# Optimization experiments

Hardware: AMD Instinct MI355X
Metric: run time of the kernel (lower is better)

## Reference

```python
import jax, jax.numpy as jnp
import numpy as np

# dims: batch, time grid, encoder length, state(y) ch, control ch (incl. time), hidden, mlp width, out ch
B, T, L_IN, S, XC, H, W, O = 64, 200, 100, 8, 16, 256, 128, 8
N_SUB = 2  # fixed Dopri5 substeps per save interval (replaces diffrax adaptive PID stepping)


def setup_inputs() -> dict:
    key = jax.random.key(0)
    ks = jax.random.split(key, 16)
    rn = lambda k, shp, sc: jax.random.normal(k, shp, dtype=jnp.float32) * sc
    return {
        "y_past": rn(ks[0], (B, L_IN, S), 1.0),
        "t": jnp.linspace(0.0, 2.0, T, dtype=jnp.float32),
        "coeffs_x": rn(ks[1], (B, T, XC - 1), 1.0),
        "gru_wih": rn(ks[2], (3 * H, S + XC), (S + XC) ** -0.5),
        "gru_whh": rn(ks[3], (3 * H, H), H ** -0.5),
        "gru_b": rn(ks[4], (3 * H,), 0.01),
        "gru_bn": rn(ks[5], (H,), 0.01),
        "mlp_w0": rn(ks[6], (W, H), H ** -0.5),
        "mlp_b0": rn(ks[7], (W,), 0.01),
        "mlp_w1": rn(ks[8], (W, W), W ** -0.5),
        "mlp_b1": rn(ks[9], (W,), 0.01),
        "mlp_w2": rn(ks[10], (H * XC, W), W ** -0.5),
        "mlp_b2": rn(ks[11], (H * XC,), 0.01),
        "ro_w": rn(ks[12], (O, H), H ** -0.5),
        "ro_b": rn(ks[13], (O,), 0.01),
        "input_length": L_IN,
    }


def _forward(y_past, t, coeffs_x, gru_wih, gru_whh, gru_b, gru_bn,
             mlp_w0, mlp_b0, mlp_w1, mlp_b1, mlp_w2, mlp_b2, ro_w, ro_b, input_length):
    L = input_length  # static python int

    def gru_cell(x, h):  # equinox GRUCell math
        ig = gru_wih @ x + gru_b
        hg = gru_whh @ h
        ir, iz, ia = jnp.split(ig, 3)
        hr, hz, hn = jnp.split(hg, 3)
        r = jax.nn.sigmoid(ir + hr)
        u = jax.nn.sigmoid(iz + hz)
        n = jnp.tanh(ia + r * (hn + gru_bn))
        return n + u * (h - n)

    def vf(z, dxdt):  # CDEFunc mlp(z).reshape(H, XC) @ dX/dt
        a = jax.nn.softplus(mlp_w0 @ z + mlp_b0)
        a = jax.nn.softplus(mlp_w1 @ a + mlp_b1)
        f = jnp.tanh(mlp_w2 @ a + mlp_b2).reshape(H, XC)
        return f @ dxdt

    def dopri5_step(z, h, dxdt):  # standard Dormand-Prince 5(4) tableau
        k1 = vf(z, dxdt)
        k2 = vf(z + h * (0.2 * k1), dxdt)
        k3 = vf(z + h * (3 / 40 * k1 + 9 / 40 * k2), dxdt)
        k4 = vf(z + h * (44 / 45 * k1 - 56 / 15 * k2 + 32 / 9 * k3), dxdt)
        k5 = vf(z + h * (19372 / 6561 * k1 - 25360 / 2187 * k2 + 64448 / 6561 * k3 - 212 / 729 * k4), dxdt)
        k6 = vf(z + h * (9017 / 3168 * k1 - 355 / 33 * k2 + 46732 / 5247 * k3 + 49 / 176 * k4 - 5103 / 18656 * k5), dxdt)
        return z + h * (35 / 384 * k1 + 500 / 1113 * k3 + 125 / 192 * k4 - 2187 / 6784 * k5 + 11 / 84 * k6)

    def single(y_p, cx):
        X = jnp.concatenate([cx, t[:, None]], axis=1)  # (T, XC): control values = linear interp knots
        enc_in = jnp.concatenate([y_p, X[:L]], axis=1)  # (L, S+XC); control.evaluate at knots == knot values
        z0, _ = jax.lax.scan(lambda h_, x: (gru_cell(x, h_), None),
                             jnp.zeros((H,), dtype=y_p.dtype), enc_in)
        t_fut = t[L:]
        X_fut = X[L:]
        dts = t_fut[1:] - t_fut[:-1]                       # (Tf-1,)
        dXdt = (X_fut[1:] - X_fut[:-1]) / dts[:, None]     # piecewise-constant derivative of linear interp

        def interval(z, inp):
            dxdt, dt_tot = inp
            hstep = dt_tot / N_SUB
            z, _ = jax.lax.scan(lambda zz, _: (dopri5_step(zz, hstep, dxdt), None), z, None, length=N_SUB)
            return z, z

        _, zs = jax.lax.scan(interval, z0, (dXdt, dts))     # (Tf-1, H)
        ys = jnp.concatenate([z0[None], zs], axis=0)        # (Tf, H), saved at t_future
        return ys @ ro_w.T + ro_b                           # readout, (Tf, O)

    return jax.vmap(single)(y_past, coeffs_x)


def reference(y_past, t, coeffs_x, gru_wih, gru_whh, gru_b, gru_bn,
              mlp_w0, mlp_b0, mlp_w1, mlp_b1, mlp_w2, mlp_b2, ro_w, ro_b, input_length):
    return _forward(y_past, t, coeffs_x, gru_wih, gru_whh, gru_b, gru_bn,
                    mlp_w0, mlp_b0, mlp_w1, mlp_b1, mlp_w2, mlp_b2, ro_w, ro_b, input_length)
```

## Files before the change

### kernel.cpp

```cpp
#include <hip/hip_runtime.h>
#include <math.h>

constexpr int B_   = 64;
constexpr int T_   = 200;
constexpr int L_IN = 100;
constexpr int S_   = 8;
constexpr int XC_  = 16;
constexpr int H_   = 256;
constexpr int W_   = 128;
constexpr int O_   = 8;
constexpr int GR_  = 3 * H_;
constexpr int HXC  = H_ * XC_;

constexpr int NB   = 4;
constexpr int ZPB  = 64;
constexpr int SLOT = 128;

#define NT 1024

constexpr size_t OFF_WIHT = 0;
constexpr size_t OFF_WHHT = OFF_WIHT + 24ull * GR_;
constexpr size_t OFF_W2T  = OFF_WHHT + (size_t)H_ * GR_;
constexpr size_t OFF_KX   = OFF_W2T + (size_t)W_ * HXC;
constexpr size_t KX_U64   = (size_t)B_ * 2 * NB * SLOT;
constexpr size_t WS_FLOATS = OFF_KX + KX_U64 * 2;

__global__ void transpose_kernel(const float* __restrict__ in, float* __restrict__ out,
                                 int R, int K) {
    int o = blockIdx.x * blockDim.x + threadIdx.x;
    if (o < R * K) {
        int k = o / R;
        int j = o - k * R;
        out[o] = in[j * K + k];
    }
}

__device__ __forceinline__ float softplus_f(float x) {
    return fmaxf(x, 0.f) + log1pf(expf(-fabsf(x)));
}
__device__ __forceinline__ float sigmoid_f(float x) {
    return 1.f / (1.f + expf(-x));
}

__global__ __launch_bounds__(NT, 4) void gru_cde_dist(
    const float* __restrict__ y_past,
    const float* __restrict__ tvals,
    const float* __restrict__ cx,
    const float* __restrict__ wih,
    const float* __restrict__ whh,
    const float* __restrict__ gru_b,
    const float* __restrict__ gru_bn,
    const float* __restrict__ w0,
    const float* __restrict__ b0,
    const float* __restrict__ w1,
    const float* __restrict__ b1,
    const float* __restrict__ w2T,
    const float* __restrict__ b2,
    const float* __restrict__ ro_w,
    const float* __restrict__ ro_b,
    unsigned long long* __restrict__ kx,
    float* __restrict__ out)
{
    const int b   = blockIdx.x & (B_ - 1);
    const int q   = blockIdx.x >> 6;
    const int tid = threadIdx.x;

    __shared__ __align__(16) float z[H_];
    __shared__ __align__(16) float zsq[ZPB];
    __shared__ float kbq[5][ZPB];
    __shared__ __align__(16) float a0s[W_];
    __shared__ __align__(16) float a1s[W_];
    __shared__ float vown[W_];
    __shared__ __align__(16) float4 red4[4][256];
    __shared__ float gsum[192];
    __shared__ float gaux[ZPB];
    __shared__ __align__(16) float xb[S_ + XC_];
    __shared__ float dxs[XC_];
    __shared__ __align__(16) float4 w2lds[4][8][256];

    int  epoch = 0;
    bool dead  = false;
    float hh   = 0.f;

    auto slotbase = [&](int qq) -> size_t {
        return (((size_t)b * 2 + (epoch & 1)) * NB + qq) * SLOT;
    };
    auto publish_u64 = [&](int elem, float v) {
        unsigned long long pk = ((unsigned long long)(unsigned)epoch << 32)
                              | (unsigned long long)__float_as_uint(v);
        __hip_atomic_store(&kx[slotbase(q) + elem], pk,
                           __ATOMIC_RELAXED, __HIP_MEMORY_SCOPE_AGENT);
    };
    auto poll_u64 = [&](int qq, int elem) -> float {
        unsigned long long pk = 0;
        int guard = 0;
        for (;;) {
            pk = __hip_atomic_load(&kx[slotbase(qq) + elem],
                                   __ATOMIC_RELAXED, __HIP_MEMORY_SCOPE_AGENT);
            if ((unsigned)(pk >> 32) >= (unsigned)epoch) break;
            if (++guard > (1 << 20)) { dead = true; break; }
        }
        return __uint_as_float((unsigned)pk);
    };

    const int   seg = tid >> 6;
    const int   l63 = tid & 63;
    const int   grow = seg * H_ + q * ZPB + l63;
    const float gbr = (tid < 192) ? gru_b[grow] : 0.f;
    const float bnr = (tid < ZPB) ? gru_bn[q * ZPB + tid] : 0.f;

    if (tid < H_) z[tid] = 0.f;
    if (tid < S_ + XC_) {
        float v;
        if (tid < S_)                v = y_past[(b * L_IN) * S_ + tid];
        else if (tid < S_ + XC_ - 1) v = cx[(b * T_) * (XC_ - 1) + (tid - S_)];
        else                         v = tvals[0];
        xb[tid] = v;
    }
    __syncthreads();

    for (int step = 0; step < L_IN; ++step) {
        if (tid < 192) {
            const float4* xr = reinterpret_cast<const float4*>(xb);
            const float4* wr = reinterpret_cast<const float4*>(wih + grow * 24);
            float ig = gbr;
            #pragma unroll
            for (int c = 0; c < 6; ++c) {
                float4 wv = wr[c], xv = xr[c];
                ig += wv.x * xv.x + wv.y * xv.y + wv.z * xv.z + wv.w * xv.w;
            }
            const float4* hr = reinterpret_cast<const float4*>(whh + grow * 256);
            const float4* z4 = reinterpret_cast<const float4*>(z);
            float hg = 0.f, hg2 = 0.f;
            #pragma unroll 8
            for (int c = 0; c < 64; c += 2) {
                float4 wa = hr[c],     za = z4[c];
                float4 wb = hr[c + 1], zb = z4[c + 1];
                hg  += wa.x * za.x + wa.y * za.y + wa.z * za.z + wa.w * za.w;
                hg2 += wb.x * zb.x + wb.y * zb.y + wb.z * zb.z + wb.w * zb.w;
            }
            hg += hg2;
            if (seg < 2) gsum[tid] = ig + hg;
            else { gsum[tid] = ig; gaux[l63] = hg; }
        }
        __syncthreads();
        epoch++;
        if (tid < ZPB) {
            float rr = sigmoid_f(gsum[tid]);
            float uu = sigmoid_f(gsum[64 + tid]);
            float nn = tanhf(gsum[128 + tid] + rr * (gaux[tid] + bnr));
            float zo = z[q * ZPB + tid];
            float znew = nn + uu * (zo - nn);
            z[q * ZPB + tid] = znew;
            publish_u64(tid, znew);
        } else if (tid < 256) {
            if (!dead) {
                int pp = tid >> 6;
                int qq = (q + pp) & 3;
                int e  = tid & 63;
                float v = poll_u64(qq, e);
                z[qq * 64 + e] = v;
            }
        } else if (tid < 256 + S_ + XC_ && step + 1 < L_IN) {
            int c = tid - 256;
            float v;
            if (c < S_)                v = y_past[(b * L_IN + step + 1) * S_ + c];
            else if (c < S_ + XC_ - 1) v = cx[(b * T_ + step + 1) * (XC_ - 1) + (c - S_)];
            else                       v = tvals[step + 1];
            xb[c] = v;
        }
        __syncthreads();
    }

    auto readout = [&](int idx) {
        if (q == 0 && tid < 8 * 64) {
            int o  = tid >> 6;
            int kk = tid & 63;
            float4 wv = reinterpret_cast<const float4*>(ro_w)[o * 64 + kk];
            float4 zv = *reinterpret_cast<const float4*>(&z[kk * 4]);
            float p = wv.x * zv.x + wv.y * zv.y + wv.z * zv.z + wv.w * zv.w;
            p += __shfl_xor(p, 1);
            p += __shfl_xor(p, 2);
            p += __shfl_xor(p, 4);
            p += __shfl_xor(p, 8);
            p += __shfl_xor(p, 16);
            p += __shfl_xor(p, 32);
            if (kk == 0) out[(b * L_IN + idx) * O_ + o] = p + ro_b[o];
        }
    };

    readout(0);

    const int wv_ = tid >> 6;
    const int ln  = tid & 63;
    const int vr  = wv_ * 8 + (ln >> 3);
    const int vc  = ln & 7;
    const int g2  = tid >> 8;
    const int u   = tid & 255;

    const float4* __restrict__ w04  = reinterpret_cast<const float4*>(w0);
    const float4* __restrict__ w14  = reinterpret_cast<const float4*>(w1);
    const float4* __restrict__ w2T4 = reinterpret_cast<const float4*>(w2T);

    const float4 w0r0 = w04[vr * 64 + q * 16 + vc * 2];
    const float4 w0r1 = w04[vr * 64 + q * 16 + vc * 2 + 1];
    const float4 w1r0 = w14[vr * 32 + vc * 4 + 0];
    const float4 w1r1 = w14[vr * 32 + vc * 4 + 1];
    const float4 w1r2 = w14[vr * 32 + vc * 4 + 2];
    const float4 w1r3 = w14[vr * 32 + vc * 4 + 3];
    const size_t w2base = (size_t)g2 * 32 * 1024 + (size_t)q * 256 + u;
    const float4 w2c0 = w2T4[w2base + 0 * 1024];
    const float4 w2c1 = w2T4[w2base + 1 * 1024];
    const float4 w2c2 = w2T4[w2base + 2 * 1024];
    const float4 w2c3 = w2T4[w2base + 3 * 1024];
    const float4 w2c4 = w2T4[w2base + 4 * 1024];
    const float4 w2c5 = w2T4[w2base + 5 * 1024];
    const float4 w2c6 = w2T4[w2base + 6 * 1024];
    const float4 w2c7 = w2T4[w2base + 7 * 1024];
    for (int it = 0; it < 8; ++it) {
        int L   = it * 1024 + tid;
        int g2l = L >> 11;
        int jl  = (L >> 8) & 7;
        int ul  = L & 255;
        w2lds[g2l][jl][ul] =
            w2T4[(size_t)(g2l * 32 + 8 + jl) * 1024 + (size_t)q * 256 + ul];
    }

    const float b0r = (tid < W_) ? b0[tid] : 0.f;
    const float b1r = b1[vr];
    float4 b2c = make_float4(0.f, 0.f, 0.f, 0.f);
    if (tid < 256) b2c = reinterpret_cast<const float4*>(b2)[q * 256 + tid];
    float4 dx4 = make_float4(0.f, 0.f, 0.f, 0.f);
    __syncthreads();

    for (int i = 0; i < T_ - L_IN - 1; ++i) {
        float dt = tvals[L_IN + i + 1] - tvals[L_IN + i];
        hh = dt * 0.5f;
        if (tid < XC_) {
            float xa, xbv;
            if (tid < XC_ - 1) {
                xa  = cx[(b * T_ + L_IN + i) * (XC_ - 1) + tid];
                xbv = cx[(b * T_ + L_IN + i + 1) * (XC_ - 1) + tid];
            } else {
                xa  = tvals[L_IN + i];
                xbv = tvals[L_IN + i + 1];
            }
            dxs[tid] = (xbv - xa) / dt;
        }
        __syncthreads();
        if (tid < 256) {
            int c0 = (tid & 3) * 4;
            dx4 = make_float4(dxs[c0], dxs[c0 + 1], dxs[c0 + 2], dxs[c0 + 3]);
        }

        for (int sub = 0; sub < 2; ++sub) {
            if (tid < ZPB) zsq[tid] = z[q * ZPB + tid];
            __syncthreads();

            for (int s = 0; s < 6; ++s) {
                epoch++;
                {
                    const float* zp = &zsq[vc * 8];
                    float pv = w0r0.x * zp[0] + w0r0.y * zp[1]
                             + w0r0.z * zp[2] + w0r0.w * zp[3]
                             + w0r1.x * zp[4] + w0r1.y * zp[5]
                             + w0r1.z * zp[6] + w0r1.w * zp[7];
                    pv += __shfl_xor(pv, 1);
                    pv += __shfl_xor(pv, 2);
                    pv += __shfl_xor(pv, 4);
                    if ((ln & 7) == 0) {
                        vown[vr] = pv;
                        publish_u64(vr, pv);
                    }
                }
                __syncthreads();
                if (tid < W_) {
                    float gv = vown[tid] + b0r;
                    if (!dead) {
                        const size_t s1 = slotbase((q + 1) & 3) + tid;
                        const size_t s2 = slotbase((q + 2) & 3) + tid;
                        const size_t s3 = slotbase((q + 3) & 3) + tid;
                        unsigned long long p1 = 0, p2 = 0, p3 = 0;
                        bool d1 = false, d2 = false, d3 = false;
                        int guard = 0;
                        do {
                            if (!d1) {
                                p1 = __hip_atomic_load(&kx[s1], __ATOMIC_RELAXED,
                                                       __HIP_MEMORY_SCOPE_AGENT);
                                d1 = (unsigned)(p1 >> 32) >= (unsigned)epoch;
                            }
                            if (!d2) {
                                p2 = __hip_atomic_load(&kx[s2], __ATOMIC_RELAXED,
                                                       __HIP_MEMORY_SCOPE_AGENT);
                                d2 = (unsigned)(p2 >> 32) >= (unsigned)epoch;
                            }
                            if (!d3) {
                                p3 = __hip_atomic_load(&kx[s3], __ATOMIC_RELAXED,
                                                       __HIP_MEMORY_SCOPE_AGENT);
                                d3 = (unsigned)(p3 >> 32) >= (unsigned)epoch;
                            }
                            if (++guard > (1 << 20)) { dead = true; break; }
                        } while (!(d1 && d2 && d3));
                        gv += __uint_as_float((unsigned)p1)
                            + __uint_as_float((unsigned)p2)
                            + __uint_as_float((unsigned)p3);
                    }
                    a0s[tid] = softplus_f(gv);
                }
                __syncthreads();
                {
                    const float4* ap = reinterpret_cast<const float4*>(a0s) + vc * 4;
                    float4 a0v = ap[0], a1v = ap[1], a2v = ap[2], a3v = ap[3];
                    float pa = w1r0.x * a0v.x + w1r0.y * a0v.y
                             + w1r0.z * a0v.z + w1r0.w * a0v.w
                             + w1r1.x * a1v.x + w1r1.y * a1v.y
                             + w1r1.z * a1v.z + w1r1.w * a1v.w
                             + w1r2.x * a2v.x + w1r2.y * a2v.y
                             + w1r2.z * a2v.z + w1r2.w * a2v.w
                             + w1r3.x * a3v.x + w1r3.y * a3v.y
                             + w1r3.z * a3v.z + w1r3.w * a3v.w;
                    pa += __shfl_xor(pa, 1);
                    pa += __shfl_xor(pa, 2);
                    pa += __shfl_xor(pa, 4);
                    if ((ln & 7) == 0) a1s[vr] = softplus_f(pa + b1r);
                }
                __syncthreads();
                {
                    const int base = g2 * 32;
                    float4 acc = make_float4(0.f, 0.f, 0.f, 0.f);
                    #define W2MAC(c_, idx_) { float av_ = a1s[base + (idx_)]; \
                        acc.x += (c_).x * av_; acc.y += (c_).y * av_; \
                        acc.z += (c_).z * av_; acc.w += (c_).w * av_; }
                    W2MAC(w2c0, 0) W2MAC(w2c1, 1) W2MAC(w2c2, 2) W2MAC(w2c3, 3)
                    W2MAC(w2c4, 4) W2MAC(w2c5, 5) W2MAC(w2c6, 6) W2MAC(w2c7, 7)
                    #pragma unroll
                    for (int jl = 0; jl < 8; ++jl) {
                        float4 wvv = w2lds[g2][jl][u];
                        float av = a1s[base + 8 + jl];
                        acc.x += wvv.x * av; acc.y += wvv.y * av;
                        acc.z += wvv.z * av; acc.w += wvv.w * av;
                    }
                    const float4* wp = w2T4 + (size_t)(base + 16) * 1024
                                     + (size_t)q * 256 + u;
                    #pragma unroll 4
                    for (int js = 0; js < 16; ++js) {
                        float4 wvv = wp[(size_t)js * 1024];
                        float av = a1s[base + 16 + js];
                        acc.x += wvv.x * av; acc.y += wvv.y * av;
                        acc.z += wvv.z * av; acc.w += wvv.w * av;
                    }
                    #undef W2MAC
                    red4[g2][u] = acc;
                }
                __syncthreads();
                if (tid < 256) {
                    float4 t0 = red4[0][tid], t1 = red4[1][tid];
                    float4 t2 = red4[2][tid], t3 = red4[3][tid];
                    float p = tanhf(t0.x + t1.x + t2.x + t3.x + b2c.x) * dx4.x
                            + tanhf(t0.y + t1.y + t2.y + t3.y + b2c.y) * dx4.y
                            + tanhf(t0.z + t1.z + t2.z + t3.z + b2c.z) * dx4.z
                            + tanhf(t0.w + t1.w + t2.w + t3.w + b2c.w) * dx4.w;
                    p += __shfl_xor(p, 1);
                    p += __shfl_xor(p, 2);
                    if ((tid & 3) == 0) {
                        int ii = tid >> 2;
                        float kv = p;
                        float zc = z[q * ZPB + ii];
                        if (s == 0) {
                            kbq[0][ii] = kv;
                            zsq[ii] = zc + hh * (0.2f * kv);
                        } else if (s == 1) {
                            kbq[1][ii] = kv;
                            zsq[ii] = zc + hh * (0.075f * kbq[0][ii] + 0.225f * kv);
                        } else if (s == 2) {
                            kbq[2][ii] = kv;
                            zsq[ii] = zc + hh * ((44.f / 45.f) * kbq[0][ii]
                                               - (56.f / 15.f) * kbq[1][ii]
                                               + (32.f / 9.f) * kv);
                        } else if (s == 3) {
                            kbq[3][ii] = kv;
                            zsq[ii] = zc + hh * ((19372.f / 6561.f) * kbq[0][ii]
                                               - (25360.f / 2187.f) * kbq[1][ii]
                                               + (64448.f / 6561.f) * kbq[2][ii]
                                               - (212.f / 729.f) * kv);
                        } else if (s == 4) {
                            kbq[4][ii] = kv;
                            zsq[ii] = zc + hh * ((9017.f / 3168.f) * kbq[0][ii]
                                               - (355.f / 33.f) * kbq[1][ii]
                                               + (46732.f / 5247.f) * kbq[2][ii]
                                               + (49.f / 176.f) * kbq[3][ii]
                                               - (5103.f / 18656.f) * kv);
                        } else {
                            z[q * ZPB + ii] = zc + hh * ((35.f / 384.f) * kbq[0][ii]
                                                       + (500.f / 1113.f) * kbq[2][ii]
                                                       + (125.f / 192.f) * kbq[3][ii]
                                                       - (2187.f / 6784.f) * kbq[4][ii]
                                                       + (11.f / 84.f) * kv);
                        }
                    }
                }
                __syncthreads();
            }
        }

        epoch++;
        if (tid < ZPB) publish_u64(tid, z[q * ZPB + tid]);
        if (q == 0 && tid >= 64 && tid < 256 && !dead) {
            int pp = tid >> 6;
            int e  = tid & 63;
            z[pp * 64 + e] = poll_u64(pp, e);
        }
        __syncthreads();
        readout(i + 1);
    }
}

__global__ __launch_bounds__(NT) void gru_cde_mono(
    const float* __restrict__ y_past, const float* __restrict__ tvals,
    const float* __restrict__ cx,
    const float* __restrict__ wih, const float* __restrict__ whh,
    const float* __restrict__ gru_b, const float* __restrict__ gru_bn,
    const float* __restrict__ w0, const float* __restrict__ b0,
    const float* __restrict__ w1, const float* __restrict__ b1,
    const float* __restrict__ w2, const float* __restrict__ b2,
    const float* __restrict__ ro_w, const float* __restrict__ ro_b,
    float* __restrict__ out)
{
    const int b   = blockIdx.x;
    const int tid = threadIdx.x;

    __shared__ __align__(16) float z[H_];
    __shared__ float zsv[H_];
    __shared__ float kbv[6][H_];
    __shared__ float a0v[W_];
    __shared__ float a1v[W_];
    __shared__ float redv[8][W_];
    __shared__ float gsum[GR_];
    __shared__ float gaux[H_];
    __shared__ float xb[S_ + XC_];
    __shared__ float dxsv[XC_];

    const float gb_t = (tid < GR_) ? gru_b[tid] : 0.f;
    const float bn_t = (tid < H_) ? gru_bn[tid] : 0.f;
    const float4 bb = reinterpret_cast<const float4*>(b2)[tid];

    if (tid < H_) z[tid] = 0.f;
    __syncthreads();

    for (int step = 0; step < L_IN; ++step) {
        if (tid < S_ + XC_) {
            float v;
            if (tid < S_)                v = y_past[(b * L_IN + step) * S_ + tid];
            else if (tid < S_ + XC_ - 1) v = cx[(b * T_ + step) * (XC_ - 1) + (tid - S_)];
            else                         v = tvals[step];
            xb[tid] = v;
        }
        __syncthreads();
        if (tid < GR_) {
            float ig = gb_t;
            #pragma unroll
            for (int k = 0; k < S_ + XC_; ++k) ig += wih[tid * (S_ + XC_) + k] * xb[k];
            float hg = 0.f;
            #pragma unroll 8
            for (int k = 0; k < H_; ++k) hg += whh[tid * H_ + k] * z[k];
            if (tid < 2 * H_) gsum[tid] = ig + hg;
            else { gsum[tid] = ig; gaux[tid - 2 * H_] = hg; }
        }
        __syncthreads();
        if (tid < H_) {
            float r = sigmoid_f(gsum[tid]);
            float u = sigmoid_f(gsum[tid + H_]);
            float n = tanhf(gsum[tid + 2 * H_] + r * (gaux[tid] + bn_t));
            z[tid] = n + u * (z[tid] - n);
        }
        __syncthreads();
    }

    auto readout = [&](int idx) {
        if (tid < 8 * 64) {
            int o  = tid >> 6;
            int kk = tid & 63;
            float4 wv = reinterpret_cast<const float4*>(ro_w)[o * 64 + kk];
            float4 zv = *reinterpret_cast<const float4*>(&z[kk * 4]);
            float p = wv.x * zv.x + wv.y * zv.y + wv.z * zv.z + wv.w * zv.w;
            p += __shfl_xor(p, 1);
            p += __shfl_xor(p, 2);
            p += __shfl_xor(p, 4);
            p += __shfl_xor(p, 8);
            p += __shfl_xor(p, 16);
            p += __shfl_xor(p, 32);
            if (kk == 0) out[(b * L_IN + idx) * O_ + o] = p + ro_b[o];
        }
    };

    readout(0);

    auto vf = [&](const float* zin, int s) {
        const int g = tid >> 7;
        const int r = tid & 127;
        {
            float acc = 0.f;
            const int k0 = g * 32;
            #pragma unroll 8
            for (int k = k0; k < k0 + 32; ++k) acc += w0[r * H_ + k] * zin[k];
            redv[g][r] = acc;
        }
        __syncthreads();
        if (tid < W_) {
            float sa = b0[tid];
            #pragma unroll
            for (int gg = 0; gg < 8; ++gg) sa += redv[gg][tid];
            a0v[tid] = softplus_f(sa);
        }
        __syncthreads();
        {
            float acc = 0.f;
            const int k0 = g * 16;
            #pragma unroll
            for (int k = k0; k < k0 + 16; ++k) acc += w1[r * W_ + k] * a0v[k];
            redv[g][r] = acc;
        }
        __syncthreads();
        if (tid < W_) {
            float sa = b1[tid];
            #pragma unroll
            for (int gg = 0; gg < 8; ++gg) sa += redv[gg][tid];
            a1v[tid] = softplus_f(sa);
        }
        __syncthreads();
        {
            float4 acc = make_float4(0.f, 0.f, 0.f, 0.f);
            const int jj = tid * 4;
            #pragma unroll 4
            for (int k = 0; k < W_; ++k) {
                float av = a1v[k];
                acc.x += w2[(jj + 0) * W_ + k] * av;
                acc.y += w2[(jj + 1) * W_ + k] * av;
                acc.z += w2[(jj + 2) * W_ + k] * av;
                acc.w += w2[(jj + 3) * W_ + k] * av;
            }
            const int c0 = jj & 15;
            float p = tanhf(acc.x + bb.x) * dxsv[c0]
                    + tanhf(acc.y + bb.y) * dxsv[c0 + 1]
                    + tanhf(acc.z + bb.z) * dxsv[c0 + 2]
                    + tanhf(acc.w + bb.w) * dxsv[c0 + 3];
            p += __shfl_xor(p, 1);
            p += __shfl_xor(p, 2);
            if ((tid & 3) == 0) kbv[s][tid >> 2] = p;
        }
        __syncthreads();
    };

    for (int i = 0; i < T_ - L_IN - 1; ++i) {
        float dt = tvals[L_IN + i + 1] - tvals[L_IN + i];
        if (tid < XC_) {
            float xa, xbv;
            if (tid < XC_ - 1) {
                xa  = cx[(b * T_ + L_IN + i) * (XC_ - 1) + tid];
                xbv = cx[(b * T_ + L_IN + i + 1) * (XC_ - 1) + tid];
            } else {
                xa  = tvals[L_IN + i];
                xbv = tvals[L_IN + i + 1];
            }
            dxsv[tid] = (xbv - xa) / dt;
        }
        const float hh = dt * 0.5f;
        __syncthreads();

        for (int sub = 0; sub < 2; ++sub) {
            vf(z, 0);
            if (tid < H_) zsv[tid] = z[tid] + hh * (0.2f * kbv[0][tid]);
            __syncthreads();
            vf(zsv, 1);
            if (tid < H_) zsv[tid] = z[tid] + hh * (0.075f * kbv[0][tid] + 0.225f * kbv[1][tid]);
            __syncthreads();
            vf(zsv, 2);
            if (tid < H_) zsv[tid] = z[tid] + hh * ((44.f / 45.f) * kbv[0][tid]
                                                - (56.f / 15.f) * kbv[1][tid]
                                                + (32.f / 9.f) * kbv[2][tid]);
            __syncthreads();
            vf(zsv, 3);
            if (tid < H_) zsv[tid] = z[tid] + hh * ((19372.f / 6561.f) * kbv[0][tid]
                                                - (25360.f / 2187.f) * kbv[1][tid]
                                                + (64448.f / 6561.f) * kbv[2][tid]
                                                - (212.f / 729.f) * kbv[3][tid]);
            __syncthreads();
            vf(zsv, 4);
            if (tid < H_) zsv[tid] = z[tid] + hh * ((9017.f / 3168.f) * kbv[0][tid]
                                                - (355.f / 33.f) * kbv[1][tid]
                                                + (46732.f / 5247.f) * kbv[2][tid]
                                                + (49.f / 176.f) * kbv[3][tid]
                                                - (5103.f / 18656.f) * kbv[4][tid]);
            __syncthreads();
            vf(zsv, 5);
            if (tid < H_) {
                z[tid] = z[tid] + hh * ((35.f / 384.f) * kbv[0][tid]
                                      + (500.f / 1113.f) * kbv[2][tid]
                                      + (125.f / 192.f) * kbv[3][tid]
                                      - (2187.f / 6784.f) * kbv[4][tid]
                                      + (11.f / 84.f) * kbv[5][tid]);
            }
            __syncthreads();
        }
        readout(i + 1);
    }
}

extern "C" void kernel_launch(void* const* d_in, const int* in_sizes, int n_in,
                              void* d_out, int out_size, void* d_ws, size_t ws_size,
                              hipStream_t stream) {
    const float* y_past = (const float*)d_in[0];
    const float* tvals  = (const float*)d_in[1];
    const float* cx     = (const float*)d_in[2];
    const float* wih    = (const float*)d_in[3];
    const float* whh    = (const float*)d_in[4];
    const float* gb     = (const float*)d_in[5];
    const float* gbn    = (const float*)d_in[6];
    const float* w0     = (const float*)d_in[7];
    const float* b0     = (const float*)d_in[8];
    const float* w1     = (const float*)d_in[9];
    const float* b1     = (const float*)d_in[10];
    const float* w2     = (const float*)d_in[11];
    const float* b2     = (const float*)d_in[12];
    const float* ro_w   = (const float*)d_in[13];
    const float* ro_b   = (const float*)d_in[14];
    float* out = (float*)d_out;

    if (ws_size >= WS_FLOATS * sizeof(float)) {
        float* ws = (float*)d_ws;
        {
            int n = HXC * W_;
            transpose_kernel<<<(n + 255) / 256, 256, 0, stream>>>(
                w2, ws + OFF_W2T, HXC, W_);
        }
        hipMemsetAsync((char*)d_ws + OFF_KX * sizeof(float), 0,
                       KX_U64 * sizeof(unsigned long long), stream);
        gru_cde_dist<<<B_ * NB, NT, 0, stream>>>(
            y_past, tvals, cx,
            wih, whh, gb, gbn,
            w0, b0, w1, b1, ws + OFF_W2T, b2,
            ro_w, ro_b,
            (unsigned long long*)(ws + OFF_KX), out);
    } else {
        gru_cde_mono<<<B_, NT, 0, stream>>>(
            y_past, tvals, cx,
            wih, whh, gb, gbn,
            w0, b0, w1, b1, w2, b2,
            ro_w, ro_b, out);
    }
}
```

Baseline: 8.546 ms.

## Reduce w2 partial sums across K-groups with wave shuffles instead of LDS

The thread-to-work mapping of the w2 matvec changes so the four K-group partial sums for one output column sit in the same wavefront (lanes differing by 16 and 32). They are now combined with cross-lane shuffles instead of being written to a shared-memory red4 buffer. This removes that LDS buffer and one block-wide barrier per RK stage, and spreads the tanh/dot epilogue across all waves instead of only the first 256 threads. The cost is extra shuffle instructions and a different w2 global and LDS access pattern, which may coalesce less well (16-float4 runs per lane group).

After: 10.06 ms. 17.8% more time.

```diff
diff --git a/kernel.cpp b/kernel.cpp
--- a/kernel.cpp
+++ b/kernel.cpp
@@ -71,7 +71,6 @@
     __shared__ __align__(16) float a0s[W_];
     __shared__ __align__(16) float a1s[W_];
     __shared__ float vown[W_];
-    __shared__ __align__(16) float4 red4[4][256];
     __shared__ float gsum[192];
     __shared__ float gaux[ZPB];
     __shared__ __align__(16) float xb[S_ + XC_];
@@ -195,8 +194,8 @@
     const int ln  = tid & 63;
     const int vr  = wv_ * 8 + (ln >> 3);
     const int vc  = ln & 7;
-    const int g2  = tid >> 8;
-    const int u   = tid & 255;
+    const int kg  = ln >> 4;
+    const int u2  = wv_ * 16 + (ln & 15);
 
     const float4* __restrict__ w04  = reinterpret_cast<const float4*>(w0);
     const float4* __restrict__ w14  = reinterpret_cast<const float4*>(w1);
@@ -208,7 +207,7 @@
     const float4 w1r1 = w14[vr * 32 + vc * 4 + 1];
     const float4 w1r2 = w14[vr * 32 + vc * 4 + 2];
     const float4 w1r3 = w14[vr * 32 + vc * 4 + 3];
-    const size_t w2base = (size_t)g2 * 32 * 1024 + (size_t)q * 256 + u;
+    const size_t w2base = (size_t)kg * 32 * 1024 + (size_t)q * 256 + u2;
     const float4 w2c0 = w2T4[w2base + 0 * 1024];
     const float4 w2c1 = w2T4[w2base + 1 * 1024];
     const float4 w2c2 = w2T4[w2base + 2 * 1024];
@@ -228,8 +227,7 @@
 
     const float b0r = (tid < W_) ? b0[tid] : 0.f;
     const float b1r = b1[vr];
-    float4 b2c = make_float4(0.f, 0.f, 0.f, 0.f);
-    if (tid < 256) b2c = reinterpret_cast<const float4*>(b2)[q * 256 + tid];
+    const float4 b2c = reinterpret_cast<const float4*>(b2)[q * 256 + u2];
     float4 dx4 = make_float4(0.f, 0.f, 0.f, 0.f);
     __syncthreads();
 
@@ -248,8 +246,8 @@
             dxs[tid] = (xbv - xa) / dt;
         }
         __syncthreads();
-        if (tid < 256) {
-            int c0 = (tid & 3) * 4;
+        {
+            int c0 = (ln & 3) * 4;
             dx4 = make_float4(dxs[c0], dxs[c0 + 1], dxs[c0 + 2], dxs[c0 + 3]);
         }
 
@@ -326,7 +324,7 @@
                 }
                 __syncthreads();
                 {
-                    const int base = g2 * 32;
+                    const int base = kg * 32;
                     float4 acc = make_float4(0.f, 0.f, 0.f, 0.f);
                     #define W2MAC(c_, idx_) { float av_ = a1s[base + (idx_)]; \
                         acc.x += (c_).x * av_; acc.y += (c_).y * av_; \
@@ -335,13 +333,13 @@
                     W2MAC(w2c4, 4) W2MAC(w2c5, 5) W2MAC(w2c6, 6) W2MAC(w2c7, 7)
                     #pragma unroll
                     for (int jl = 0; jl < 8; ++jl) {
-                        float4 wvv = w2lds[g2][jl][u];
+                        float4 wvv = w2lds[kg][jl][u2];
                         float av = a1s[base + 8 + jl];
                         acc.x += wvv.x * av; acc.y += wvv.y * av;
                         acc.z += wvv.z * av; acc.w += wvv.w * av;
                     }
                     const float4* wp = w2T4 + (size_t)(base + 16) * 1024
-                                     + (size_t)q * 256 + u;
+                                     + (size_t)q * 256 + u2;
                     #pragma unroll 4
                     for (int js = 0; js < 16; ++js) {
                         float4 wvv = wp[(size_t)js * 1024];
@@ -350,20 +348,18 @@
                         acc.z += wvv.z * av; acc.w += wvv.w * av;
                     }
                     #undef W2MAC
-                    red4[g2][u] = acc;
-                }
-                __syncthreads();
-                if (tid < 256) {
-                    float4 t0 = red4[0][tid], t1 = red4[1][tid];
-                    float4 t2 = red4[2][tid], t3 = red4[3][tid];
-                    float p = tanhf(t0.x + t1.x + t2.x + t3.x + b2c.x) * dx4.x
-                            + tanhf(t0.y + t1.y + t2.y + t3.y + b2c.y) * dx4.y
-                            + tanhf(t0.z + t1.z + t2.z + t3.z + b2c.z) * dx4.z
-                            + tanhf(t0.w + t1.w + t2.w + t3.w + b2c.w) * dx4.w;
+                    acc.x += __shfl_xor(acc.x, 16); acc.y += __shfl_xor(acc.y, 16);
+                    acc.z += __shfl_xor(acc.z, 16); acc.w += __shfl_xor(acc.w, 16);
+                    acc.x += __shfl_xor(acc.x, 32); acc.y += __shfl_xor(acc.y, 32);
+                    acc.z += __shfl_xor(acc.z, 32); acc.w += __shfl_xor(acc.w, 32);
+                    float p = tanhf(acc.x + b2c.x) * dx4.x
+                            + tanhf(acc.y + b2c.y) * dx4.y
+                            + tanhf(acc.z + b2c.z) * dx4.z
+                            + tanhf(acc.w + b2c.w) * dx4.w;
                     p += __shfl_xor(p, 1);
                     p += __shfl_xor(p, 2);
-                    if ((tid & 3) == 0) {
-                        int ii = tid >> 2;
+                    if (ln < 16 && (ln & 3) == 0) {
+                        int ii = wv_ * 4 + (ln >> 2);
                         float kv = p;
                         float zc = z[q * ZPB + ii];
                         if (s == 0) {
```
